# Kernel optimization log

Measured on AMD Instinct MI355X. Metric: run time of the kernel, lower is better.

## Reference

```python
import jax, jax.numpy as jnp
import numpy as np

HEAD_NUM = 8


def setup_inputs() -> dict:
    key = jax.random.key(0)
    k1, k2, k3, k4 = jax.random.split(key, 4)
    B, S, F = 16, 512, 512
    H = HEAD_NUM
    x = jax.random.normal(k1, (B, S, F), dtype=jnp.float32)
    # keras initializer 'normal' ~ small random normal weights
    wq = jax.random.normal(k2, (F, S * H), dtype=jnp.float32) * 0.05
    wk = jax.random.normal(k3, (F, S * H), dtype=jnp.float32) * 0.05
    wv = jax.random.normal(k4, (F, S * H), dtype=jnp.float32) * 0.05
    return {"x": x, "wq": wq, "wk": wk, "wv": wv}


def _split_heads(t, H):
    # tf.stack(tf.split(t, H, axis=2)): [B,S,H*S] -> [H,B,S,S]
    B, S, D = t.shape
    return t.reshape(B, S, H, D // H).transpose(2, 0, 1, 3)


def reference(x, wq, wk, wv):
    H = HEAD_NUM
    B, S, F = x.shape
    q = _split_heads(jnp.einsum('bsf,fd->bsd', x, wq), H)  # [H,B,S,S]
    k = _split_heads(jnp.einsum('bsf,fd->bsd', x, wk), H)
    v = _split_heads(jnp.einsum('bsf,fd->bsd', x, wv), H)
    # NOTE: no 1/sqrt(d) scaling in the original module
    scores = jax.nn.softmax(jnp.einsum('hbid,hbjd->hbij', q, k), axis=-1)
    eff = jnp.einsum('hbij,hbjd->hbid', scores, v)  # [H,B,S,S]
    # tf.concat(tf.split(eff, H), axis=-1) + squeeze: [H,B,S,S] -> [B,S,H*S]
    return eff.transpose(1, 2, 0, 3).reshape(B, S, H * S)
```

## Files before the change

### kernel.cpp

```cpp
#include <hip/hip_runtime.h>


typedef unsigned short u16;
typedef __bf16 bf16x8 __attribute__((ext_vector_type(8)));
typedef unsigned short u16x4 __attribute__((ext_vector_type(4)));
typedef unsigned short u16x8s __attribute__((ext_vector_type(8)));
typedef float f32x4 __attribute__((ext_vector_type(4)));

typedef __attribute__((address_space(1))) void gvoid_t;
typedef __attribute__((address_space(3))) void svoid_t;

__device__ __forceinline__ u16 f2bf(float f) {
  unsigned u = __float_as_uint(f);
  u = (u + 0x7fffu + ((u >> 16) & 1u)) >> 16;
  return (u16)u;
}
__device__ __forceinline__ float bf2f(u16 h) {
  return __uint_as_float(((unsigned)h) << 16);
}

__device__ __forceinline__ f32x4 mfma16(bf16x8 a, bf16x8 b, f32x4 c) {
  return __builtin_amdgcn_mfma_f32_16x16x32_bf16(a, b, c, 0, 0, 0);
}

__global__ __launch_bounds__(256) void split_hl_kernel(
    const float* __restrict__ in, u16* __restrict__ hi, u16* __restrict__ lo,
    int n4) {
  int i = blockIdx.x * 256 + threadIdx.x;
  if (i >= n4) return;
  float4 v = ((const float4*)in)[i];
  float vv[4] = {v.x, v.y, v.z, v.w};
  u16x4 h, l;
#pragma unroll
  for (int j = 0; j < 4; ++j) {
    u16 hh = f2bf(vv[j]);
    h[j] = hh;
    l[j] = f2bf(vv[j] - bf2f(hh));
  }
  ((u16x4*)hi)[i] = h;
  ((u16x4*)lo)[i] = l;
}

__global__ __launch_bounds__(256) void transpose_split_w(
    const float* __restrict__ in, u16* __restrict__ hi, u16* __restrict__ lo) {
  __shared__ float t[32][33];
  int d0 = blockIdx.x * 32, f0 = blockIdx.y * 32;
  int tx = threadIdx.x, ty = threadIdx.y;
#pragma unroll
  for (int r = 0; r < 4; ++r)
    t[ty + r * 8][tx] = in[(size_t)(f0 + ty + r * 8) * 4096 + d0 + tx];
  __syncthreads();
#pragma unroll
  for (int r = 0; r < 4; ++r) {
    float v = t[tx][ty + r * 8];
    int d = d0 + ty + r * 8, f = f0 + tx;
    u16 h = f2bf(v);
    size_t idx = (size_t)d * 512 + f;
    hi[idx] = h;
    lo[idx] = f2bf(v - bf2f(h));
  }
}

__device__ __forceinline__ bf16x8 ldsfrag(const u16* tile, int row, int quad) {
  int c = quad ^ ((row >> 1) & 3);
  return *(const bf16x8*)(tile + row * 32 + c * 8);
}

__device__ __forceinline__ void stage_tile(u16* ldsTile, const u16* g0, int ld,
                                           int wave, int lane) {
#pragma unroll
  for (int r = 0; r < 2; ++r) {
    int p = r * 256 + wave * 64 + lane;
    int m = p >> 2;
    int cq = (p & 3) ^ ((m >> 1) & 3);
    const u16* g = g0 + (size_t)m * ld + cq * 8;
    u16* l = ldsTile + (size_t)(r * 256 + wave * 64) * 8;
    __builtin_amdgcn_global_load_lds((gvoid_t*)g, (svoid_t*)l, 16, 0, 0);
  }
}

template <int SPLIT, int OMODE>
__global__ __launch_bounds__(256, 2) void gemm_bt(
    const u16* __restrict__ Ah, const u16* __restrict__ Al,
    const u16* __restrict__ Bh, const u16* __restrict__ Bl,
    void* __restrict__ C0, void* __restrict__ C1, int lda, int ldb, int ldc,
    int K, size_t aH, size_t aB, size_t bH, size_t bB, size_t cH, size_t cB) {
  __shared__ __align__(16) u16 lds[(SPLIT ? 4 : 2) * 4096];
  u16* lAh = lds;
  u16* lAl = SPLIT ? (lds + 4096) : lds;
  u16* lBh = lds + (SPLIT ? 8192 : 4096);
  u16* lBl = SPLIT ? (lds + 12288) : lds;

  const int zh = blockIdx.z >> 4, zb = blockIdx.z & 15;
  Ah += zh * aH + zb * aB;
  Al += zh * aH + zb * aB;
  Bh += zh * bH + zb * bB;
  Bl += zh * bH + zb * bB;
  const size_t cOff = zh * cH + zb * cB;

  const int m0 = blockIdx.y * 128, n0 = blockIdx.x * 128;
  const int tid = threadIdx.x;
  const int wave = tid >> 6, lane = tid & 63;
  const int quad = lane >> 4, l16 = lane & 15;
  const int wm = (wave >> 1) * 64, wn = (wave & 1) * 64;

  f32x4 acc[4][4] = {};

  for (int k0 = 0; k0 < K; k0 += 32) {
    stage_tile(lAh, Ah + (size_t)m0 * lda + k0, lda, wave, lane);
    if (SPLIT) stage_tile(lAl, Al + (size_t)m0 * lda + k0, lda, wave, lane);
    stage_tile(lBh, Bh + (size_t)n0 * ldb + k0, ldb, wave, lane);
    if (SPLIT) stage_tile(lBl, Bl + (size_t)n0 * ldb + k0, ldb, wave, lane);
    __syncthreads();

    bf16x8 a_h[4], a_l[4], b_h[4], b_l[4];
#pragma unroll
    for (int i = 0; i < 4; ++i) {
      a_h[i] = ldsfrag(lAh, wm + i * 16 + l16, quad);
      b_h[i] = ldsfrag(lBh, wn + i * 16 + l16, quad);
      if (SPLIT) {
        a_l[i] = ldsfrag(lAl, wm + i * 16 + l16, quad);
        b_l[i] = ldsfrag(lBl, wn + i * 16 + l16, quad);
      }
    }
#pragma unroll
    for (int i = 0; i < 4; ++i)
#pragma unroll
      for (int j = 0; j < 4; ++j) {
        acc[i][j] = mfma16(a_h[i], b_h[j], acc[i][j]);
        if (SPLIT) {
          acc[i][j] = mfma16(a_h[i], b_l[j], acc[i][j]);
          acc[i][j] = mfma16(a_l[i], b_h[j], acc[i][j]);
        }
      }
    __syncthreads();
  }

#pragma unroll
  for (int i = 0; i < 4; ++i) {
#pragma unroll
    for (int j = 0; j < 4; ++j) {
      int col = n0 + wn + j * 16 + l16;
#pragma unroll
      for (int r = 0; r < 4; ++r) {
        int row = m0 + wm + i * 16 + quad * 4 + r;
        size_t idx = cOff + (size_t)row * ldc + col;
        float v = acc[i][j][r];
        if (OMODE == 0) {
          ((float*)C0)[idx] = v;
        } else if (OMODE == 1) {
          ((u16*)C0)[idx] = f2bf(v);
        } else {
          u16 h = f2bf(v);
          ((u16*)C0)[idx] = h;
          ((u16*)C1)[idx] = f2bf(v - bf2f(h));
        }
      }
    }
  }
}

__device__ __forceinline__ void stage256(u16* tile, const u16* g0, int ld,
                                         int tid) {
  const int wave = tid >> 6;
#pragma unroll
  for (int r = 0; r < 2; ++r) {
    int p = r * 512 + tid;
    int m = p >> 2;
    int cq = (p & 3) ^ ((m >> 1) & 3);
    const u16* g = g0 + (size_t)m * ld + cq * 8;
    u16* l = tile + (size_t)(r * 512 + wave * 64) * 8;
    __builtin_amdgcn_global_load_lds((gvoid_t*)g, (svoid_t*)l, 16, 0, 0);
  }
}

template <int SPLIT>
__device__ __forceinline__ void stage_all256(u16* buf, const u16* Ah,
                                             const u16* Al, const u16* Bh,
                                             const u16* Bl, int lda, int ldb,
                                             int m0, int n0, int k0, int tid) {
  stage256(buf, Ah + (size_t)m0 * lda + k0, lda, tid);
  if (SPLIT) stage256(buf + 8192, Al + (size_t)m0 * lda + k0, lda, tid);
  stage256(buf + (SPLIT ? 16384 : 8192), Bh + (size_t)n0 * ldb + k0, ldb, tid);
  if (SPLIT) stage256(buf + 24576, Bl + (size_t)n0 * ldb + k0, ldb, tid);
}

template <int SPLIT, int OMODE>
__global__ __launch_bounds__(512, 2) void gemm256(
    const u16* __restrict__ Ah, const u16* __restrict__ Al,
    const u16* __restrict__ Bh, const u16* __restrict__ Bl,
    void* __restrict__ C0, void* __restrict__ C1, int lda, int ldb, int ldc,
    int K, size_t aH, size_t aB, size_t bH, size_t bB, size_t cH, size_t cB) {
  constexpr int BUF = (SPLIT ? 4 : 2) * 8192;
  __shared__ __align__(16) u16 lds[2 * BUF];

  const int gx = gridDim.x, gy = gridDim.y;
  const int nb = gx * gy * (int)gridDim.z;
  int orig = blockIdx.x + gx * (blockIdx.y + gy * blockIdx.z);
  int swz = orig;
  if ((nb & 7) == 0) swz = (orig & 7) * (nb >> 3) + (orig >> 3);
  const int bx = swz % gx;
  const int byz = swz / gx;
  const int by = byz % gy;
  const int bz = byz / gy;

  const int zh = bz >> 4, zb = bz & 15;
  Ah += zh * aH + zb * aB;
  Al += zh * aH + zb * aB;
  Bh += zh * bH + zb * bB;
  Bl += zh * bH + zb * bB;
  const size_t cOff = zh * cH + zb * cB;

  const int m0 = by * 256, n0 = bx * 256;
  const int tid = threadIdx.x;
  const int wave = tid >> 6, lane = tid & 63;
  const int quad = lane >> 4, l16 = lane & 15;
  const int wm = (wave >> 2) * 128, wn = (wave & 3) * 64;

  f32x4 acc[8][4] = {};

  stage_all256<SPLIT>(lds, Ah, Al, Bh, Bl, lda, ldb, m0, n0, 0, tid);
  __syncthreads();

  int cur = 0;
  for (int k0 = 0; k0 < K; k0 += 32) {
    if (k0 + 32 < K)
      stage_all256<SPLIT>(lds + (cur ^ 1) * BUF, Ah, Al, Bh, Bl, lda, ldb, m0,
                          n0, k0 + 32, tid);

    u16* lA_h = lds + cur * BUF;
    u16* lA_l = lA_h + 8192;
    u16* lB_h = lA_h + (SPLIT ? 16384 : 8192);
    u16* lB_l = lA_h + 24576;

    bf16x8 bhf[4], blf[4];
#pragma unroll
    for (int j = 0; j < 4; ++j) {
      bhf[j] = ldsfrag(lB_h, wn + j * 16 + l16, quad);
      if (SPLIT) blf[j] = ldsfrag(lB_l, wn + j * 16 + l16, quad);
    }
#pragma unroll
    for (int i = 0; i < 8; ++i) {
      bf16x8 ah = ldsfrag(lA_h, wm + i * 16 + l16, quad);
      bf16x8 al;
      if (SPLIT) al = ldsfrag(lA_l, wm + i * 16 + l16, quad);
#pragma unroll
      for (int j = 0; j < 4; ++j) {
        acc[i][j] = mfma16(ah, bhf[j], acc[i][j]);
        if (SPLIT) {
          acc[i][j] = mfma16(ah, blf[j], acc[i][j]);
          acc[i][j] = mfma16(al, bhf[j], acc[i][j]);
        }
      }
    }
    __syncthreads();
    cur ^= 1;
  }

#pragma unroll
  for (int i = 0; i < 8; ++i) {
#pragma unroll
    for (int j = 0; j < 4; ++j) {
      int col = n0 + wn + j * 16 + l16;
#pragma unroll
      for (int r = 0; r < 4; ++r) {
        int row = m0 + wm + i * 16 + quad * 4 + r;
        size_t idx = cOff + (size_t)row * ldc + col;
        float v = acc[i][j][r];
        if (OMODE == 0) {
          ((float*)C0)[idx] = v;
        } else if (OMODE == 1) {
          ((u16*)C0)[idx] = f2bf(v);
        } else {
          u16 h = f2bf(v);
          ((u16*)C0)[idx] = h;
          ((u16*)C1)[idx] = f2bf(v - bf2f(h));
        }
      }
    }
  }
}

__global__ __launch_bounds__(512, 2) void logits_sm(
    const u16* __restrict__ Th, const u16* __restrict__ Tl,
    const u16* __restrict__ Xh, const u16* __restrict__ Xl,
    u16* __restrict__ P, int lda, int ldb,
    size_t aH, size_t aB, size_t bB, size_t cH, size_t cB) {
  __shared__ __align__(16) u16 lds[81920];

  const int gx = gridDim.x;
  const int nb = gx * (int)gridDim.y;
  int orig = blockIdx.x + gx * blockIdx.y;
  int swz = orig;
  if ((nb & 7) == 0) swz = (orig & 7) * (nb >> 3) + (orig >> 3);
  const int by = swz % gx;
  const int bz = swz / gx;

  const int zh = bz >> 4, zb = bz & 15;
  const u16* gA_h = Th + zh * aH + zb * aB;
  const u16* gA_l = Tl + zh * aH + zb * aB;
  const u16* gB_h = Xh + zb * bB;
  const u16* gB_l = Xl + zb * bB;
  const size_t cOff = zh * cH + zb * cB;

  const int m0 = by * 128;
  const int tid = threadIdx.x;
  const int wave = tid >> 6, lane = tid & 63;
  const int quad = lane >> 4, l16 = lane & 15;
  const int wn = wave * 64;

  const u16* A_h = gA_h + (size_t)m0 * lda;
  const u16* A_l = gA_l + (size_t)m0 * lda;

  f32x4 acc[8][4] = {};

  auto STAGE = [&](int b, int kk) {
    u16* d = lds + b * 40960;
    {
      int m = tid >> 2;
      int cq = (tid & 3) ^ ((m >> 1) & 3);
      u16* l0 = d + (size_t)(wave * 64) * 8;
      __builtin_amdgcn_global_load_lds(
          (gvoid_t*)(A_h + (size_t)m * lda + kk + cq * 8), (svoid_t*)l0, 16, 0,
          0);
      __builtin_amdgcn_global_load_lds(
          (gvoid_t*)(A_l + (size_t)m * lda + kk + cq * 8),
          (svoid_t*)(l0 + 4096 * 8 / 8 + 0), 16, 0, 0);
    }
#pragma unroll
    for (int r = 0; r < 4; ++r) {
      int p = r * 512 + tid;
      int m = p >> 2;
      int cq = (p & 3) ^ ((m >> 1) & 3);
      u16* l0 = d + 8192 + (size_t)(r * 512 + wave * 64) * 8;
      __builtin_amdgcn_global_load_lds(
          (gvoid_t*)(gB_h + (size_t)m * ldb + kk + cq * 8), (svoid_t*)l0, 16,
          0, 0);
      __builtin_amdgcn_global_load_lds(
          (gvoid_t*)(gB_l + (size_t)m * ldb + kk + cq * 8),
          (svoid_t*)(l0 + 16384), 16, 0, 0);
    }
  };

  STAGE(0, 0);
  __syncthreads();

  int cur = 0;
  for (int t = 0; t < 16; ++t) {
    if (t + 1 < 16) STAGE(cur ^ 1, (t + 1) * 32);

    u16* buf = lds + cur * 40960;
    u16* lA_h = buf;
    u16* lA_l = buf + 4096;
    u16* lB_h = buf + 8192;
    u16* lB_l = buf + 24576;

    bf16x8 bhf[4], blf[4];
#pragma unroll
    for (int j = 0; j < 4; ++j) {
      bhf[j] = ldsfrag(lB_h, wn + j * 16 + l16, quad);
      blf[j] = ldsfrag(lB_l, wn + j * 16 + l16, quad);
    }
#pragma unroll
    for (int i = 0; i < 8; ++i) {
      bf16x8 ah = ldsfrag(lA_h, i * 16 + l16, quad);
      bf16x8 al = ldsfrag(lA_l, i * 16 + l16, quad);
#pragma unroll
      for (int j = 0; j < 4; ++j) {
        acc[i][j] = mfma16(ah, bhf[j], acc[i][j]);
        acc[i][j] = mfma16(ah, blf[j], acc[i][j]);
        acc[i][j] = mfma16(al, bhf[j], acc[i][j]);
      }
    }
    __syncthreads();
    cur ^= 1;
  }

  float* smax = (float*)lds;
  float* ssum = (float*)(lds + 2048);

#pragma unroll
  for (int i = 0; i < 8; ++i)
#pragma unroll
    for (int r = 0; r < 4; ++r) {
      float m = fmaxf(fmaxf(acc[i][0][r], acc[i][1][r]),
                      fmaxf(acc[i][2][r], acc[i][3][r]));
#pragma unroll
      for (int o = 1; o < 16; o <<= 1) m = fmaxf(m, __shfl_xor(m, o));
      if (l16 == 0) smax[(i * 16 + quad * 4 + r) * 8 + wave] = m;
    }
  __syncthreads();

#pragma unroll
  for (int i = 0; i < 8; ++i)
#pragma unroll
    for (int r = 0; r < 4; ++r) {
      int row = i * 16 + quad * 4 + r;
      f32x4 a = *(f32x4*)&smax[row * 8];
      f32x4 b = *(f32x4*)&smax[row * 8 + 4];
      float m = fmaxf(fmaxf(fmaxf(a[0], a[1]), fmaxf(a[2], a[3])),
                      fmaxf(fmaxf(b[0], b[1]), fmaxf(b[2], b[3])));
      float s = 0.f;
#pragma unroll
      for (int j = 0; j < 4; ++j) {
        float e = __expf(acc[i][j][r] - m);
        acc[i][j][r] = e;
        s += e;
      }
#pragma unroll
      for (int o = 1; o < 16; o <<= 1) s += __shfl_xor(s, o);
      if (l16 == 0) ssum[row * 8 + wave] = s;
    }
  __syncthreads();

#pragma unroll
  for (int i = 0; i < 8; ++i)
#pragma unroll
    for (int r = 0; r < 4; ++r) {
      int row = i * 16 + quad * 4 + r;
      f32x4 a = *(f32x4*)&ssum[row * 8];
      f32x4 b = *(f32x4*)&ssum[row * 8 + 4];
      float s = (a[0] + a[1]) + (a[2] + a[3]) + (b[0] + b[1]) + (b[2] + b[3]);
      float inv = 1.0f / s;
      size_t base = cOff + (size_t)(m0 + row) * 512;
#pragma unroll
      for (int j = 0; j < 4; ++j)
        P[base + wn + j * 16 + l16] = f2bf(acc[i][j][r] * inv);
    }
}

extern "C" void kernel_launch(void* const* d_in, const int* in_sizes, int n_in,
                              void* d_out, int out_size, void* d_ws,
                              size_t ws_size, hipStream_t stream) {
  const float* x = (const float*)d_in[0];
  const float* wq = (const float*)d_in[1];
  const float* wk = (const float*)d_in[2];
  const float* wv = (const float*)d_in[3];
  float* out = (float*)d_out;
  char* ws = (char*)d_ws;

  const size_t MB = 1024ull * 1024ull;
  u16* XHI = (u16*)(ws + 0 * MB);
  u16* XLO = (u16*)(ws + 8 * MB);
  u16* WQH = (u16*)(ws + 16 * MB);
  u16* WQL = (u16*)(ws + 20 * MB);
  u16* WKH = (u16*)(ws + 24 * MB);
  u16* WKL = (u16*)(ws + 28 * MB);
  u16* WVTH = (u16*)(ws + 32 * MB);
  u16* WVTL = (u16*)(ws + 36 * MB);
  u16* MPH = (u16*)(ws + 40 * MB);
  u16* MPL = (u16*)(ws + 44 * MB);
  u16* THI = (u16*)(ws + 48 * MB);
  u16* TLO = (u16*)(ws + 112 * MB);
  u16* VT = (u16*)(ws + 176 * MB);
  u16* P = THI;

  split_hl_kernel<<<4096, 256, 0, stream>>>(x, XHI, XLO, 1048576);
  split_hl_kernel<<<2048, 256, 0, stream>>>(wq, WQH, WQL, 524288);
  split_hl_kernel<<<2048, 256, 0, stream>>>(wk, WKH, WKL, 524288);
  transpose_split_w<<<dim3(128, 16), dim3(32, 8), 0, stream>>>(wv, WVTH, WVTL);

  gemm_bt<1, 2><<<dim3(4, 4, 8), 256, 0, stream>>>(
      WKH, WKL, WQH, WQL, MPH, MPL, 4096, 4096, 512, 512,
       0,  512,  0,  512,  0,  262144);

  gemm256<1, 2><<<dim3(2, 32, 8), 512, 0, stream>>>(
      XHI, XLO, MPH, MPL, THI, TLO, 512, 512, 512, 512,
      0, 0, 0, 262144, 0, 4194304);

  gemm256<0, 1><<<dim3(32, 16, 1), 512, 0, stream>>>(
      WVTH, WVTH, XHI, XHI, VT, nullptr, 512, 512, 8192, 512,
      0, 0, 0, 0, 0, 0);

  logits_sm<<<dim3(4, 128), 512, 0, stream>>>(
      THI, TLO, XHI, XLO, P, 512, 512,
       4194304,  262144,  262144,
       4194304,  262144);

  gemm256<0, 0><<<dim3(2, 2, 128), 512, 0, stream>>>(
      P, P, VT, VT, out, nullptr, 512, 8192, 4096, 512,
       4194304,  262144,  4194304,  512,
       512,  2097152);
}
```

Baseline: 499.1 us.

## Fuse softmax probabilities with PV matmul inside logits kernel

The logits+softmax kernel now keeps the normalized probabilities for its 128-row tile in LDS as bf16 and multiplies them directly by V (register-prefetched, staged into LDS per 32-wide k step), writing fp32 output. This removes the bf16 P write to global memory, its reread, and the separate PV GEMM launch. In exchange each block does the full 512-wide PV work with a serial 16-step loop, and the extra accumulators raise register pressure. V is re-read by each of the four row blocks.

```diff
diff --git a/kernel.cpp b/kernel.cpp
--- a/kernel.cpp
+++ b/kernel.cpp
@@ -281,11 +281,11 @@
   }
 }
 
-__global__ __launch_bounds__(512, 2) void logits_sm(
+__global__ __launch_bounds__(512, 2) void logits_sm_pv(
     const u16* __restrict__ Th, const u16* __restrict__ Tl,
     const u16* __restrict__ Xh, const u16* __restrict__ Xl,
-    u16* __restrict__ P, int lda, int ldb,
-    size_t aH, size_t aB, size_t bB, size_t cH, size_t cB) {
+    const u16* __restrict__ VT, float* __restrict__ out,
+    size_t aH, size_t aB, size_t bB) {
   __shared__ __align__(16) u16 lds[81920];
 
   const int gx = gridDim.x;
@@ -301,13 +301,14 @@
   const u16* gA_l = Tl + zh * aH + zb * aB;
   const u16* gB_h = Xh + zb * bB;
   const u16* gB_l = Xl + zb * bB;
-  const size_t cOff = zh * cH + zb * cB;
+  const u16* gV = VT + (size_t)zh * 512 * 8192 + (size_t)zb * 512;
 
   const int m0 = by * 128;
   const int tid = threadIdx.x;
   const int wave = tid >> 6, lane = tid & 63;
   const int quad = lane >> 4, l16 = lane & 15;
   const int wn = wave * 64;
+  const int lda = 512, ldb = 512;
 
   const u16* A_h = gA_h + (size_t)m0 * lda;
   const u16* A_l = gA_l + (size_t)m0 * lda;
@@ -325,7 +326,7 @@
           0);
       __builtin_amdgcn_global_load_lds(
           (gvoid_t*)(A_l + (size_t)m * lda + kk + cq * 8),
-          (svoid_t*)(l0 + 4096 * 8 / 8 + 0), 16, 0, 0);
+          (svoid_t*)(l0 + 4096), 16, 0, 0);
     }
 #pragma unroll
     for (int r = 0; r < 4; ++r) {
@@ -422,10 +423,73 @@
       f32x4 b = *(f32x4*)&ssum[row * 8 + 4];
       float s = (a[0] + a[1]) + (a[2] + a[3]) + (b[0] + b[1]) + (b[2] + b[3]);
       float inv = 1.0f / s;
-      size_t base = cOff + (size_t)(m0 + row) * 512;
-#pragma unroll
-      for (int j = 0; j < 4; ++j)
-        P[base + wn + j * 16 + l16] = f2bf(acc[i][j][r] * inv);
+#pragma unroll
+      for (int j = 0; j < 4; ++j) acc[i][j][r] *= inv;
+    }
+  __syncthreads();
+
+  u16* Plds = lds;
+  u16* Vbuf = lds + 65536;
+
+  u16x8s vreg[4];
+  auto VLOAD = [&](int kk) {
+#pragma unroll
+    for (int r = 0; r < 4; ++r) {
+      int p = r * 512 + tid;
+      int m = p >> 2;
+      int cq = (p & 3) ^ ((m >> 1) & 3);
+      vreg[r] = *(const u16x8s*)(gV + (size_t)m * 8192 + kk + cq * 8);
+    }
+  };
+  VLOAD(0);
+
+#pragma unroll
+  for (int i = 0; i < 8; ++i)
+#pragma unroll
+    for (int j = 0; j < 4; ++j)
+#pragma unroll
+      for (int r = 0; r < 4; ++r) {
+        int row = i * 16 + quad * 4 + r;
+        int col = wn + j * 16 + l16;
+        int t = col >> 5, c = col & 31;
+        int cp = (c >> 3) ^ ((row >> 1) & 3);
+        Plds[t * 4096 + row * 32 + cp * 8 + (c & 7)] = f2bf(acc[i][j][r]);
+      }
+  __syncthreads();
+
+  f32x4 acc2[8][4] = {};
+  for (int t = 0; t < 16; ++t) {
+#pragma unroll
+    for (int r = 0; r < 4; ++r)
+      *(u16x8s*)(Vbuf + (size_t)(r * 512 + tid) * 8) = vreg[r];
+    if (t + 1 < 16) VLOAD((t + 1) * 32);
+    __syncthreads();
+
+    const u16* Pt = Plds + t * 4096;
+    bf16x8 bhf[4];
+#pragma unroll
+    for (int j = 0; j < 4; ++j)
+      bhf[j] = ldsfrag(Vbuf, wn + j * 16 + l16, quad);
+#pragma unroll
+    for (int i = 0; i < 8; ++i) {
+      bf16x8 pa = ldsfrag(Pt, i * 16 + l16, quad);
+#pragma unroll
+      for (int j = 0; j < 4; ++j) acc2[i][j] = mfma16(pa, bhf[j], acc2[i][j]);
+    }
+    __syncthreads();
+  }
+
+  const size_t oBase = ((size_t)zb * 512 + m0) * 4096 + (size_t)zh * 512;
+#pragma unroll
+  for (int i = 0; i < 8; ++i)
+#pragma unroll
+    for (int j = 0; j < 4; ++j) {
+      int col = wn + j * 16 + l16;
+#pragma unroll
+      for (int r = 0; r < 4; ++r) {
+        int row = i * 16 + quad * 4 + r;
+        out[oBase + (size_t)row * 4096 + col] = acc2[i][j][r];
+      }
     }
 }
 
@@ -453,7 +517,6 @@
   u16* THI = (u16*)(ws + 48 * MB);
   u16* TLO = (u16*)(ws + 112 * MB);
   u16* VT = (u16*)(ws + 176 * MB);
-  u16* P = THI;
 
   split_hl_kernel<<<4096, 256, 0, stream>>>(x, XHI, XLO, 1048576);
   split_hl_kernel<<<2048, 256, 0, stream>>>(wq, WQH, WQL, 524288);
@@ -472,13 +535,7 @@
       WVTH, WVTH, XHI, XHI, VT, nullptr, 512, 512, 8192, 512,
       0, 0, 0, 0, 0, 0);
 
-  logits_sm<<<dim3(4, 128), 512, 0, stream>>>(
-      THI, TLO, XHI, XLO, P, 512, 512,
-       4194304,  262144,  262144,
-       4194304,  262144);
-
-  gemm256<0, 0><<<dim3(2, 2, 128), 512, 0, stream>>>(
-      P, P, VT, VT, out, nullptr, 512, 8192, 4096, 512,
-       4194304,  262144,  4194304,  512,
-       512,  2097152);
-}
+  logits_sm_pv<<<dim3(4, 128), 512, 0, stream>>>(
+      THI, TLO, XHI, XLO, VT, out,
+       4194304,  262144,  262144);
+}
```

Result: no change. 496.2 us (-0.6%).
